# Kernel optimization log

Measured on AMD Instinct MI355X. Metric: run time of the kernel, lower is better.

The kernel has to match this reference:

```python
import jax, jax.numpy as jnp
from jax import lax
import numpy as np


def _bn(x, g, b, eps=1e-5):
    # BatchNorm2d in training mode: biased batch stats over (N,H,W) per channel
    m = jnp.mean(x, axis=(0, 2, 3), keepdims=True)
    v = jnp.mean((x - m) ** 2, axis=(0, 2, 3), keepdims=True)
    return (x - m) * lax.rsqrt(v + eps) * g[None, :, None, None] + b[None, :, None, None]


def _conv(x, w, b, pad):
    y = lax.conv_general_dilated(x, w, (1, 1), [(pad, pad), (pad, pad)],
                                 dimension_numbers=('NCHW', 'OIHW', 'NCHW'))
    return y + b[None, :, None, None]


def _prelu(x, a):
    return jnp.where(x >= 0, x, a * x)


def _maxpool2(x):
    return lax.reduce_window(x, -jnp.inf, lax.max, (1, 1, 2, 2), (1, 1, 2, 2), 'VALID')


def _up2(x):
    # UpsamplingBilinear2d(scale_factor=2) -> bilinear, align_corners=True
    B, C, H, W = x.shape
    def idx(n):
        pos = jnp.arange(2 * n, dtype=x.dtype) * (n - 1) / (2 * n - 1)
        lo = jnp.floor(pos).astype(jnp.int32)
        hi = jnp.minimum(lo + 1, n - 1)
        return lo, hi, pos - lo.astype(x.dtype)
    lo, hi, f = idx(H)
    x = x[:, :, lo, :] * (1 - f)[:, None] + x[:, :, hi, :] * f[:, None]
    lo, hi, f = idx(W)
    x = x[:, :, :, lo] * (1 - f) + x[:, :, :, hi] * f
    return x


def _forward(x, n16, sigma16, bias16, prelu_a,
             bn3_g, bn3_b, bn32_g, bn32_b, bn64_g, bn64_b, bn128_g, bn128_b,
             w1, b1, w2, b2, w3, b3, w4, b4, w5, b5, w6, b6, w7, b7, w11, b11):
    B, C, H, W = x.shape
    # 16 enhancement curves fused: r_k = x^{n_k} / (x^{n_k} + sigma_k^{n_k} + bias_k)
    xn = x[None] ** n16[:, None, None, None, None]          # (16,B,3,H,W)
    r = xn / (xn + (sigma16 ** n16)[:, None, None, None, None]
              + bias16[:, None, None, None, None])
    # each branch gets its own BatchNorm2d(3) stats (same affine params)
    r = jax.vmap(lambda t: _bn(t, bn3_g, bn3_b))(r)
    x_fusion = jnp.transpose(r, (1, 0, 2, 3, 4)).reshape(B, 16 * C, H, W)
    x1 = _bn(_maxpool2(_prelu(_conv(x_fusion, w1, b1, 1), prelu_a)), bn32_g, bn32_b)
    x2 = _bn(_maxpool2(_prelu(_conv(x1, w2, b2, 1), prelu_a)), bn64_g, bn64_b)
    x3 = _bn(_maxpool2(_prelu(_conv(x2, w3, b3, 1), prelu_a)), bn128_g, bn128_b)
    x4 = _bn(_conv(x3, w4, b4, 1), bn128_g, bn128_b)
    x5 = _bn(_up2(_prelu(_conv(jnp.concatenate([x4, x3], 1), w5, b5, 1), prelu_a)), bn64_g, bn64_b)
    x6 = _bn(_up2(_prelu(_conv(jnp.concatenate([x2, x5], 1), w6, b6, 1), prelu_a)), bn32_g, bn32_b)
    x_out = jax.nn.sigmoid(_up2(_prelu(_conv(jnp.concatenate([x1, x6], 1), w7, b7, 1), prelu_a)))
    x_out = _conv(x_out, w11, b11, 0)
    x_mean = jnp.mean(x, axis=1, keepdims=True)
    x_out1 = jnp.mean(x_out, axis=1, keepdims=True)
    return x_out1 * (x / (x_mean + 1e-6))


def setup_inputs() -> dict:
    key = jax.random.key(0)
    ks = jax.random.split(key, 16)
    B, H, W = 8, 256, 256
    nf = 32
    x = jax.random.uniform(ks[0], (B, 3, H, W), jnp.float32, 1e-3, 1.0)
    n16 = jnp.arange(1, 17, dtype=jnp.float32) * 0.5
    sigma16 = jnp.full((16,), 0.5, jnp.float32)
    bias16 = jnp.full((16,), 1e-4, jnp.float32)
    prelu_a = jnp.float32(0.25)
    def cw(k, o, i, kk):
        return jax.random.normal(k, (o, i, kk, kk), jnp.float32) * 0.05
    def cb(o):
        return jnp.zeros((o,), jnp.float32)
    return dict(
        x=x, n16=n16, sigma16=sigma16, bias16=bias16, prelu_a=prelu_a,
        bn3_g=jnp.ones((3,), jnp.float32), bn3_b=jnp.zeros((3,), jnp.float32),
        bn32_g=jnp.ones((32,), jnp.float32), bn32_b=jnp.zeros((32,), jnp.float32),
        bn64_g=jnp.ones((64,), jnp.float32), bn64_b=jnp.zeros((64,), jnp.float32),
        bn128_g=jnp.ones((128,), jnp.float32), bn128_b=jnp.zeros((128,), jnp.float32),
        w1=cw(ks[1], nf, 48, 3), b1=cb(nf),
        w2=cw(ks[2], 2 * nf, nf, 3), b2=cb(2 * nf),
        w3=cw(ks[3], 4 * nf, 2 * nf, 3), b3=cb(4 * nf),
        w4=cw(ks[4], 4 * nf, 4 * nf, 3), b4=cb(4 * nf),
        w5=cw(ks[5], 2 * nf, 8 * nf, 3), b5=cb(2 * nf),
        w6=cw(ks[6], nf, 4 * nf, 3), b6=cb(nf),
        w7=cw(ks[7], nf, 2 * nf, 3), b7=cb(nf),
        w11=cw(ks[8], 3, nf, 1), b11=cb(3),
    )


def reference(x, n16, sigma16, bias16, prelu_a,
              bn3_g, bn3_b, bn32_g, bn32_b, bn64_g, bn64_b, bn128_g, bn128_b,
              w1, b1, w2, b2, w3, b3, w4, b4, w5, b5, w6, b6, w7, b7, w11, b11):
    return _forward(x, n16, sigma16, bias16, prelu_a,
                    bn3_g, bn3_b, bn32_g, bn32_b, bn64_g, bn64_b, bn128_g, bn128_b,
                    w1, b1, w2, b2, w3, b3, w4, b4, w5, b5, w6, b6, w7, b7, w11, b11)
```

## Files before the change

kernel.cpp:

```cpp
#include <hip/hip_runtime.h>

#define FAST_EXP2(x) __builtin_amdgcn_exp2f(x)
#define FAST_LOG2(x) __builtin_amdgcn_logf(x)
#define FAST_RCP(x)  __builtin_amdgcn_rcpf(x)

static constexpr size_t S3_SUM=0,   S3_SQ=48;
static constexpr size_t S32A_SUM=96,  S32A_SQ=128;
static constexpr size_t S64A_SUM=160, S64A_SQ=224;
static constexpr size_t S128A_SUM=288,S128A_SQ=416;
static constexpr size_t S128B_SUM=544,S128B_SQ=672;
static constexpr size_t S64B_SUM=800, S64B_SQ=864;
static constexpr size_t S32B_SUM=928, S32B_SQ=960;
static constexpr size_t SPB_=2016, WBAR_=2032, BBAR_=2064;
static constexpr size_t T1_=4096;
static constexpr size_t T2_=T1_+4194304;
static constexpr size_t T3_=T2_+2097152;
static constexpr size_t T4_=T3_+1048576;
static constexpr size_t C5_=T4_+1048576;
static constexpr size_t U5_=C5_+524288;
static constexpr size_t C6_=U5_+2097152;
static constexpr size_t U6_=C6_+1048576;
static constexpr size_t C7_=U6_+4194304;
static constexpr size_t W1S_=C7_+4194304;
static constexpr size_t B1S_=W1S_+13824;
static constexpr size_t PAD_=B1S_+64;

__device__ inline void bn_ab(const float* __restrict__ sum, const float* __restrict__ sq,
                             const float* __restrict__ g, const float* __restrict__ bb,
                             float invN, int c, float& a, float& b)
{
    float m   = sum[c]*invN;
    float var = fmaxf(sq[c]*invN - m*m, 0.f);
    float inv = rsqrtf(var + 1e-5f);
    a = g[c]*inv;
    b = bb[c] - m*a;
}

__global__ __launch_bounds__(256) void k_branch_stats(
    const float* __restrict__ x, const float* __restrict__ n16,
    const float* __restrict__ sig16, const float* __restrict__ b16,
    float* __restrict__ sum, float* __restrict__ sq)
{
    const int c = blockIdx.x >> 9;
    const int chunk = blockIdx.x & 511;
    float nk[16], den[16];
#pragma unroll
    for (int k = 0; k < 16; ++k) { nk[k] = n16[k]; den[k] = powf(sig16[k], nk[k]) + b16[k]; }
    float s[16], q[16];
#pragma unroll
    for (int k = 0; k < 16; ++k) { s[k] = 0.f; q[k] = 0.f; }
    const int per = 1024;
    int start = chunk * per;
    for (int i = start + (int)threadIdx.x; i < start + per; i += 256) {
        int b = i >> 16, hw = i & 65535;
        float xv = x[(size_t)(b*3 + c)*65536 + hw];
        float t = FAST_LOG2(xv);
#pragma unroll
        for (int k = 0; k < 16; ++k) {
            float v = FAST_EXP2(nk[k]*t);
            float r = v * FAST_RCP(v + den[k]);
            s[k] += r; q[k] += r*r;
        }
    }
    __shared__ float red[4][32];
    int lane = threadIdx.x & 63, wid = threadIdx.x >> 6;
#pragma unroll
    for (int k = 0; k < 16; ++k) {
#pragma unroll
        for (int off = 32; off > 0; off >>= 1) {
            s[k] += __shfl_down(s[k], off);
            q[k] += __shfl_down(q[k], off);
        }
    }
    if (lane == 0) {
#pragma unroll
        for (int k = 0; k < 16; ++k) { red[wid][k] = s[k]; red[wid][16+k] = q[k]; }
    }
    __syncthreads();
    if (threadIdx.x < 32) {
        float v = red[0][threadIdx.x] + red[1][threadIdx.x] + red[2][threadIdx.x] + red[3][threadIdx.x];
        int k = threadIdx.x & 15;
        if (threadIdx.x < 16) atomicAdd(&sum[k*3 + c], v);
        else                  atomicAdd(&sq[k*3 + c], v);
    }
}

__global__ __launch_bounds__(256) void k_stats(
    const float* __restrict__ in, int C, int HW, int nchunks, int per,
    float* __restrict__ sum, float* __restrict__ sq)
{
    int c = blockIdx.x / nchunks;
    int chunk = blockIdx.x - c*nchunks;
    float s = 0.f, q = 0.f;
    int start = chunk * per, end = start + per;
    for (int i = start + (int)threadIdx.x; i < end; i += 256) {
        int b = i / HW, hw = i - b*HW;
        float v = in[((size_t)b*C + c)*HW + hw];
        s += v; q += v*v;
    }
#pragma unroll
    for (int off = 32; off > 0; off >>= 1) { s += __shfl_down(s, off); q += __shfl_down(q, off); }
    __shared__ float ss[4], qq[4];
    int lane = threadIdx.x & 63, wid = threadIdx.x >> 6;
    if (lane == 0) { ss[wid] = s; qq[wid] = q; }
    __syncthreads();
    if (threadIdx.x == 0) {
        atomicAdd(&sum[c], ss[0]+ss[1]+ss[2]+ss[3]);
        atomicAdd(&sq[c],  qq[0]+qq[1]+qq[2]+qq[3]);
    }
}

__global__ __launch_bounds__(256) void k_fill(
    float* __restrict__ out, const float* __restrict__ bias, int C, int HW, int total)
{
    int idx = blockIdx.x*256 + threadIdx.x;
    if (idx < total) {
        int c = (idx / HW) % C;
        out[idx] = bias[c];
    }
}

__global__ __launch_bounds__(256) void k_prep_all(
    const float* __restrict__ s3sum, const float* __restrict__ s3sq,
    const float* __restrict__ bn3_g, const float* __restrict__ bn3_b,
    const float* __restrict__ n16, const float* __restrict__ sig16, const float* __restrict__ b16,
    const float* __restrict__ w11, const float* __restrict__ b11,
    const float* __restrict__ w1, const float* __restrict__ b1,
    float* __restrict__ w1s, float* __restrict__ b1s, float* __restrict__ padg,
    float* __restrict__ spb, float* __restrict__ wbar, float* __restrict__ bbar)
{
    __shared__ float a3[48], b3[48];
    int tid = threadIdx.x;
    if (tid < 48) {
        float m   = s3sum[tid]*(1.f/524288.f);
        float var = fmaxf(s3sq[tid]*(1.f/524288.f) - m*m, 0.f);
        float inv = rsqrtf(var + 1e-5f);
        float a   = bn3_g[tid % 3]*inv;
        a3[tid] = a;
        b3[tid] = bn3_b[tid % 3] - m*a;
    }
    if (tid < 16) spb[tid] = powf(sig16[tid], n16[tid]) + b16[tid];
    else if (tid >= 64 && tid < 96) { int j = tid - 64; wbar[j] = (w11[j] + w11[32+j] + w11[64+j]) * (1.f/3.f); }
    else if (tid == 96) bbar[0] = (b11[0] + b11[1] + b11[2]) * (1.f/3.f);
    __syncthreads();
    if (tid < 48) padg[tid] = -b3[tid] * FAST_RCP(a3[tid]);
    for (int t = tid; t < 13824; t += 256) {
        int ci = (t / 9) % 48;
        w1s[t] = w1[t] * a3[ci];
    }
    if (tid < 32) {
        float s = b1[tid];
        const float* wp = w1 + tid*432;
        for (int i = 0; i < 432; ++i) s += wp[i] * b3[i/9];
        b1s[tid] = s;
    }
}

template<int COG>
__device__ inline void stats_reduceN(float (&ssum)[COG], float (&ssq)[COG],
                                     float (*redst)[2*COG], int cob,
                                     float* __restrict__ gsum, float* __restrict__ gsq)
{
    int lane = threadIdx.x & 63, wid = threadIdx.x >> 6;
#pragma unroll
    for (int co = 0; co < COG; ++co) {
#pragma unroll
        for (int off = 32; off > 0; off >>= 1) {
            ssum[co] += __shfl_down(ssum[co], off);
            ssq[co]  += __shfl_down(ssq[co],  off);
        }
    }
    if (lane == 0) {
#pragma unroll
        for (int co = 0; co < COG; ++co) { redst[wid][co] = ssum[co]; redst[wid][COG+co] = ssq[co]; }
    }
    __syncthreads();
    if (threadIdx.x < 2*COG) {
        float v = redst[0][threadIdx.x] + redst[1][threadIdx.x] + redst[2][threadIdx.x] + redst[3][threadIdx.x];
        if ((int)threadIdx.x < COG) atomicAdd(&gsum[cob + threadIdx.x], v);
        else                        atomicAdd(&gsq[cob + threadIdx.x - COG], v);
    }
}

template<int COG>
__global__ __launch_bounds__(256,2) void k_conv1f(
    const float* __restrict__ x,
    const float* __restrict__ n16, const float* __restrict__ spb,
    const float* __restrict__ w1s, const float* __restrict__ b1s,
    const float* __restrict__ padg,
    const float* __restrict__ prelu_a,
    float* __restrict__ out, float* __restrict__ gsum, float* __restrict__ gsq)
{
    const int tx = threadIdx.x & 15, ty = threadIdx.x >> 4;
    const int nco = 32 / COG;
    const int b = blockIdx.z / nco, cob = (blockIdx.z - b*nco)*COG;
    const int x0 = blockIdx.x*32, y0 = blockIdx.y*32;

    __shared__ float wl[COG*48*9];
    __shared__ float rl[2][3*1224];
    __shared__ float nl16[16], dl16[16], padl[48];
    __shared__ float redst[4][2*COG];

    for (int t = threadIdx.x; t < COG*48*9; t += 256) {
        int co = t % COG; int rest = t / COG;
        int kk = rest % 9; int ci = rest / 9;
        wl[t] = w1s[(((size_t)(cob+co))*48 + ci)*9 + kk];
    }
    if (threadIdx.x < 16)       nl16[threadIdx.x]    = n16[threadIdx.x];
    else if (threadIdx.x < 32)  dl16[threadIdx.x-16] = spb[threadIdx.x-16];
    else if (threadIdx.x < 80)  padl[threadIdx.x-32] = padg[threadIdx.x-32];

    float tlr[14];
    int off_[14]; int chpack = 0; int okf = 0;
#pragma unroll
    for (int j = 0; j < 14; ++j) {
        int i = threadIdx.x + 256*j;
        if (i < 3468) {
            int ch = i / 1156, jj = i - ch*1156;
            int rr = jj / 34, cc = jj - rr*34;
            int gy = y0 - 1 + rr, gx = x0 - 1 + cc;
            bool ok = (unsigned)gy < 256u && (unsigned)gx < 256u;
            off_[j] = ch*1224 + rr*36 + cc;
            chpack |= ch << (2*j);
            tlr[j] = 0.f;
            if (ok) {
                okf |= 1 << j;
                tlr[j] = FAST_LOG2(x[((size_t)(b*3+ch))*65536 + gy*256 + gx]);
            }
        } else { off_[j] = 3671; tlr[j] = 0.f; }
    }

    float acc[COG][4];
#pragma unroll
    for (int i = 0; i < COG; ++i)
#pragma unroll
        for (int j = 0; j < 4; ++j) acc[i][j] = 0.f;

    {
        float nk = nl16[0], dk = dl16[0];
#pragma unroll
        for (int j = 0; j < 14; ++j) {
            int ch = (chpack >> (2*j)) & 3;
            float pv = padl[ch];
            float v = FAST_EXP2(nk * tlr[j]);
            float rv = v * FAST_RCP(v + dk);
            rl[0][off_[j]] = ((okf >> j) & 1) ? rv : pv;
        }
    }
    __syncthreads();

#pragma unroll 1
    for (int k = 0; k < 16; ++k) {
        if (k < 15) {
            float nk = nl16[k+1], dk = dl16[k+1];
#pragma unroll
            for (int j = 0; j < 14; ++j) {
                int ch = (chpack >> (2*j)) & 3;
                float pv = padl[(k+1)*3 + ch];
                float v = FAST_EXP2(nk * tlr[j]);
                float rv = v * FAST_RCP(v + dk);
                rl[(k+1)&1][off_[j]] = ((okf >> j) & 1) ? rv : pv;
            }
        }
        const float* rbuf = rl[k&1];
#pragma unroll
        for (int ch = 0; ch < 3; ++ch) {
            const float* tlp = rbuf + ch*1224 + (2*ty)*36 + 2*tx;
            float iv[4][4];
#pragma unroll
            for (int r = 0; r < 4; ++r) {
                float2 a2 = *(const float2*)(tlp + r*36);
                float2 b2 = *(const float2*)(tlp + r*36 + 2);
                iv[r][0]=a2.x; iv[r][1]=a2.y; iv[r][2]=b2.x; iv[r][3]=b2.y;
            }
            const float* wbase = &wl[((k*3+ch)*9)*COG];
#pragma unroll
            for (int kh = 0; kh < 3; ++kh)
#pragma unroll
            for (int kw = 0; kw < 3; ++kw) {
                const int kk = kh*3 + kw;
                float wv[COG];
#pragma unroll
                for (int q = 0; q < COG/4; ++q) {
                    float4 wq = *((const float4*)(wbase + kk*COG) + q);
                    wv[4*q+0]=wq.x; wv[4*q+1]=wq.y; wv[4*q+2]=wq.z; wv[4*q+3]=wq.w;
                }
#pragma unroll
                for (int co = 0; co < COG; ++co)
#pragma unroll
                    for (int py = 0; py < 2; ++py)
#pragma unroll
                        for (int px = 0; px < 2; ++px)
                            acc[co][py*2+px] += wv[co]*iv[py+kh][px+kw];
            }
        }
        __syncthreads();
    }

    float a = __ldg(prelu_a);
    int pyp = (y0 >> 1) + ty, pxp = (x0 >> 1) + tx;
    float ssum[COG], ssq[COG];
#pragma unroll
    for (int co = 0; co < COG; ++co) {
        float bv = b1s[cob + co];
        float v0 = acc[co][0] + bv, v1 = acc[co][1] + bv;
        float v2 = acc[co][2] + bv, v3 = acc[co][3] + bv;
        v0 = v0 >= 0.f ? v0 : a*v0; v1 = v1 >= 0.f ? v1 : a*v1;
        v2 = v2 >= 0.f ? v2 : a*v2; v3 = v3 >= 0.f ? v3 : a*v3;
        float m = fmaxf(fmaxf(v0,v1), fmaxf(v2,v3));
        out[(((size_t)b*32 + cob + co)*128 + pyp)*128 + pxp] = m;
        ssum[co] = m; ssq[co] = m*m;
    }
    __syncthreads();
    stats_reduceN<COG>(ssum, ssq, redst, cob, gsum, gsq);
}

template<int COG, int MAXCI, bool POOL, bool SPLIT, bool STATS>
__global__ __launch_bounds__(256, (COG<=8) ? 4 : 2) void k_conv32(
    const float* __restrict__ in1, int C1,
    const float* __restrict__ sum1, const float* __restrict__ sq1,
    const float* __restrict__ g1, const float* __restrict__ bb1, float invN1,
    const float* __restrict__ in2, int C2,
    const float* __restrict__ sum2, const float* __restrict__ sq2,
    const float* __restrict__ g2, const float* __restrict__ bb2, float invN2,
    const float* __restrict__ w, const float* __restrict__ bias,
    int Cout, int H, int W, const float* __restrict__ prelu_a, int do_prelu,
    int ciN, int nsplit,
    float* __restrict__ out, float* __restrict__ gsum, float* __restrict__ gsq)
{
    const int Cin = C1 + C2;
    const int tx = threadIdx.x & 15, ty = threadIdx.x >> 4;
    const int nco = Cout / COG;
    int z = blockIdx.z;
    const int sp = z % nsplit; z /= nsplit;
    const int b = z / nco, cob = (z - b*nco)*COG;
    const int ci0 = sp * ciN;
    const int x0 = blockIdx.x*32, y0 = blockIdx.y*32;

    __shared__ float wl[COG*MAXCI*9];
    __shared__ float tile[2][34*36];
    __shared__ float redst[4][2*COG];

    for (int t = threadIdx.x; t < COG*ciN*9; t += 256) {
        int co = t % COG; int rest = t / COG;
        int k = rest % 9; int ci = rest / 9;
        wl[t] = w[(((size_t)(cob+co))*Cin + ci0 + ci)*9 + k];
    }

    float acc[COG][4];
#pragma unroll
    for (int i = 0; i < COG; ++i)
#pragma unroll
        for (int j = 0; j < 4; ++j) acc[i][j] = 0.f;

#pragma unroll 1
    for (int cb = 0; cb < ciN; cb += 2) {
#pragma unroll
        for (int sub = 0; sub < 2; ++sub) {
            int ci = ci0 + cb + sub;
            const float* in; int cc; int Cn;
            const float* sm; const float* sqp; const float* gg; const float* bbp; float iN;
            if (ci < C1) { in = in1; cc = ci;      Cn = C1; sm = sum1; sqp = sq1; gg = g1; bbp = bb1; iN = invN1; }
            else         { in = in2; cc = ci - C1; Cn = C2; sm = sum2; sqp = sq2; gg = g2; bbp = bb2; iN = invN2; }
            float scv = 1.f, shv = 0.f;
            if (sm) bn_ab(sm, sqp, gg, bbp, iN, cc, scv, shv);
            const float* base = in + ((size_t)b*Cn + cc)*H*W;
#pragma unroll 1
            for (int i = threadIdx.x; i < 34*34; i += 256) {
                int r = i / 34, c = i - r*34;
                int gy = y0 - 1 + r, gx = x0 - 1 + c;
                float v = 0.f;
                if ((unsigned)gy < (unsigned)H && (unsigned)gx < (unsigned)W)
                    v = base[(size_t)gy*W + gx]*scv + shv;
                tile[sub][r*36 + c] = v;
            }
        }
        __syncthreads();
#pragma unroll
        for (int sub = 0; sub < 2; ++sub) {
            const float* tl = &tile[sub][(2*ty)*36 + 2*tx];
            float iv[4][4];
#pragma unroll
            for (int r = 0; r < 4; ++r) {
                float2 a2 = *(const float2*)(tl + r*36);
                float2 b2 = *(const float2*)(tl + r*36 + 2);
                iv[r][0]=a2.x; iv[r][1]=a2.y; iv[r][2]=b2.x; iv[r][3]=b2.y;
            }
            const float* wbase = &wl[(cb+sub)*9*COG];
#pragma unroll
            for (int kh = 0; kh < 3; ++kh)
#pragma unroll
            for (int kw = 0; kw < 3; ++kw) {
                const int k = kh*3 + kw;
                float wv[COG];
#pragma unroll
                for (int q = 0; q < COG/4; ++q) {
                    float4 wq = *((const float4*)(wbase + k*COG) + q);
                    wv[4*q+0]=wq.x; wv[4*q+1]=wq.y; wv[4*q+2]=wq.z; wv[4*q+3]=wq.w;
                }
#pragma unroll
                for (int co = 0; co < COG; ++co)
#pragma unroll
                    for (int py = 0; py < 2; ++py)
#pragma unroll
                        for (int px = 0; px < 2; ++px)
                            acc[co][py*2+px] += wv[co]*iv[py+kh][px+kw];
            }
        }
        __syncthreads();
    }

    if (SPLIT) {
        int oy = y0 + 2*ty, ox = x0 + 2*tx;
#pragma unroll
        for (int co = 0; co < COG; ++co) {
            float* op = out + (((size_t)b*Cout + cob + co)*H + oy)*W + ox;
            atomicAdd(&op[0],     acc[co][0]);
            atomicAdd(&op[1],     acc[co][1]);
            atomicAdd(&op[W],     acc[co][2]);
            atomicAdd(&op[W + 1], acc[co][3]);
        }
    } else {
        float a = __ldg(prelu_a);
        float ssum[COG], ssq[COG];
        if (POOL) {
            const int Hp = H >> 1, Wp = W >> 1;
            int pyp = (y0 >> 1) + ty, pxp = (x0 >> 1) + tx;
#pragma unroll
            for (int co = 0; co < COG; ++co) {
                float bv = bias[cob + co];
                float v0 = acc[co][0] + bv, v1 = acc[co][1] + bv;
                float v2 = acc[co][2] + bv, v3 = acc[co][3] + bv;
                v0 = v0 >= 0.f ? v0 : a*v0; v1 = v1 >= 0.f ? v1 : a*v1;
                v2 = v2 >= 0.f ? v2 : a*v2; v3 = v3 >= 0.f ? v3 : a*v3;
                float m = fmaxf(fmaxf(v0,v1), fmaxf(v2,v3));
                out[(((size_t)b*Cout + cob + co)*Hp + pyp)*Wp + pxp] = m;
                ssum[co] = m; ssq[co] = m*m;
            }
            if (STATS) stats_reduceN<COG>(ssum, ssq, redst, cob, gsum, gsq);
        } else {
            int oy = y0 + 2*ty, ox = x0 + 2*tx;
#pragma unroll
            for (int co = 0; co < COG; ++co) {
                float bv = bias[cob + co];
                float* op = out + (((size_t)b*Cout + cob + co)*H + oy)*W + ox;
                float v0 = acc[co][0] + bv, v1 = acc[co][1] + bv;
                float v2 = acc[co][2] + bv, v3 = acc[co][3] + bv;
                if (do_prelu) {
                    v0 = v0 >= 0.f ? v0 : a*v0; v1 = v1 >= 0.f ? v1 : a*v1;
                    v2 = v2 >= 0.f ? v2 : a*v2; v3 = v3 >= 0.f ? v3 : a*v3;
                }
                op[0] = v0; op[1] = v1; op[W] = v2; op[W+1] = v3;
                ssum[co] = v0+v1+v2+v3; ssq[co] = v0*v0+v1*v1+v2*v2+v3*v3;
            }
            if (STATS) stats_reduceN<COG>(ssum, ssq, redst, cob, gsum, gsq);
        }
    }
}

__global__ __launch_bounds__(256) void k_up2(
    const float* __restrict__ in, float* __restrict__ out, int C, int h, int w,
    const float* __restrict__ prelu_a, int do_prelu,
    float* __restrict__ gsum, float* __restrict__ gsq)
{
    int idx = blockIdx.x*256 + threadIdx.x;
    int W2 = 2*w, H2 = 2*h;
    float a = do_prelu ? __ldg(prelu_a) : 0.f;
    int ox = idx % W2; int t = idx / W2; int oy = t % H2; int bc = t / H2;
    float py = ((float)oy * (float)(h-1)) / (float)(2*h - 1);
    int ly = (int)floorf(py); int hy = min(ly+1, h-1); float fy = py - (float)ly;
    float px = ((float)ox * (float)(w-1)) / (float)(2*w - 1);
    int lx = (int)floorf(px); int hx = min(lx+1, w-1); float fx = px - (float)lx;
    const float* p = in + (size_t)bc*h*w;
    float v00 = p[(size_t)ly*w + lx], v01 = p[(size_t)ly*w + hx];
    float v10 = p[(size_t)hy*w + lx], v11 = p[(size_t)hy*w + hx];
    if (do_prelu) {
        v00 = v00 >= 0.f ? v00 : a*v00;
        v01 = v01 >= 0.f ? v01 : a*v01;
        v10 = v10 >= 0.f ? v10 : a*v10;
        v11 = v11 >= 0.f ? v11 : a*v11;
    }
    float v0 = v00*(1.f-fx) + v01*fx;
    float v1 = v10*(1.f-fx) + v11*fx;
    float v = v0*(1.f-fy) + v1*fy;
    out[idx] = v;
    float s = v, q = v*v;
#pragma unroll
    for (int off = 32; off > 0; off >>= 1) { s += __shfl_down(s, off); q += __shfl_down(q, off); }
    __shared__ float ss[4], qq[4];
    int lane = threadIdx.x & 63, wid = threadIdx.x >> 6;
    if (lane == 0) { ss[wid] = s; qq[wid] = q; }
    __syncthreads();
    if (threadIdx.x == 0) {
        int c = bc % C;
        atomicAdd(&gsum[c], ss[0]+ss[1]+ss[2]+ss[3]);
        atomicAdd(&gsq[c],  qq[0]+qq[1]+qq[2]+qq[3]);
    }
}

__global__ __launch_bounds__(256) void k_final(
    const float* __restrict__ c7, const float* __restrict__ x,
    const float* __restrict__ wbar, const float* __restrict__ bbar,
    float* __restrict__ out)
{
    int idx = blockIdx.x*256 + threadIdx.x;
    if (idx >= 8*65536) return;
    int hw = idx & 65535, b = idx >> 16;
    int oy = hw >> 8, ox = hw & 255;
    float py = ((float)oy * 127.f) / 255.f;
    int ly = (int)floorf(py); int hy = min(ly+1, 127); float fy = py - (float)ly;
    float px = ((float)ox * 127.f) / 255.f;
    int lx = (int)floorf(px); int hx = min(lx+1, 127); float fx = px - (float)lx;
    float w00 = (1.f-fy)*(1.f-fx), w01 = (1.f-fy)*fx, w10 = fy*(1.f-fx), w11v = fy*fx;
    const float* base = c7 + (size_t)b*32*16384;
    float accum = bbar[0];
#pragma unroll 8
    for (int j = 0; j < 32; ++j) {
        const float* p = base + (size_t)j*16384;
        float v = p[ly*128 + lx]*w00 + p[ly*128 + hx]*w01 + p[hy*128 + lx]*w10 + p[hy*128 + hx]*w11v;
        float s = FAST_RCP(1.f + __expf(-v));
        accum += wbar[j]*s;
    }
    size_t xb = (size_t)b*3*65536 + hw;
    float x0 = x[xb], x1 = x[xb + 65536], x2 = x[xb + 2*65536];
    float m = (x0 + x1 + x2)*(1.f/3.f) + 1e-6f;
    float sc = accum * FAST_RCP(m);
    out[xb]            = sc*x0;
    out[xb + 65536]    = sc*x1;
    out[xb + 2*65536]  = sc*x2;
}

extern "C" void kernel_launch(void* const* d_in, const int* in_sizes, int n_in,
                              void* d_out, int out_size, void* d_ws, size_t ws_size,
                              hipStream_t stream) {
    const float* x       = (const float*)d_in[0];
    const float* n16     = (const float*)d_in[1];
    const float* sig16   = (const float*)d_in[2];
    const float* bia16   = (const float*)d_in[3];
    const float* prelu_a = (const float*)d_in[4];
    const float* bn3_g   = (const float*)d_in[5];
    const float* bn3_b   = (const float*)d_in[6];
    const float* bn32_g  = (const float*)d_in[7];
    const float* bn32_b  = (const float*)d_in[8];
    const float* bn64_g  = (const float*)d_in[9];
    const float* bn64_b  = (const float*)d_in[10];
    const float* bn128_g = (const float*)d_in[11];
    const float* bn128_b = (const float*)d_in[12];
    const float* w1 = (const float*)d_in[13]; const float* b1 = (const float*)d_in[14];
    const float* w2 = (const float*)d_in[15]; const float* b2 = (const float*)d_in[16];
    const float* w3 = (const float*)d_in[17]; const float* b3 = (const float*)d_in[18];
    const float* w4 = (const float*)d_in[19]; const float* b4 = (const float*)d_in[20];
    const float* w5 = (const float*)d_in[21]; const float* b5 = (const float*)d_in[22];
    const float* w6 = (const float*)d_in[23]; const float* b6 = (const float*)d_in[24];
    const float* w7 = (const float*)d_in[25]; const float* b7 = (const float*)d_in[26];
    const float* w11= (const float*)d_in[27]; const float* b11= (const float*)d_in[28];
    float* ws  = (float*)d_ws;
    float* out = (float*)d_out;

    (void)hipMemsetAsync(d_ws, 0, 4096*sizeof(float), stream);

    k_branch_stats<<<1536, 256, 0, stream>>>(x, n16, sig16, bia16, ws+S3_SUM, ws+S3_SQ);
    k_prep_all<<<1, 256, 0, stream>>>(ws+S3_SUM, ws+S3_SQ, bn3_g, bn3_b, n16, sig16, bia16,
                                      w11, b11, w1, b1,
                                      ws+W1S_, ws+B1S_, ws+PAD_, ws+SPB_, ws+WBAR_, ws+BBAR_);

    k_conv1f<8><<<dim3(8,8,32), 256, 0, stream>>>(x, n16, ws+SPB_, ws+W1S_, ws+B1S_, ws+PAD_,
                                                  prelu_a, ws+T1_, ws+S32A_SUM, ws+S32A_SQ);

    k_conv32<16,32,true,false,true><<<dim3(4,4,32), 256, 0, stream>>>(
        ws+T1_, 32, ws+S32A_SUM, ws+S32A_SQ, bn32_g, bn32_b, 1.f/131072.f,
        nullptr, 0, nullptr, nullptr, nullptr, nullptr, 0.f,
        w2, b2, 64, 128, 128, prelu_a, 1, 32, 1, ws+T2_, ws+S64A_SUM, ws+S64A_SQ);

    k_conv32<8,64,true,false,true><<<dim3(2,2,128), 256, 0, stream>>>(
        ws+T2_, 64, ws+S64A_SUM, ws+S64A_SQ, bn64_g, bn64_b, 1.f/32768.f,
        nullptr, 0, nullptr, nullptr, nullptr, nullptr, 0.f,
        w3, b3, 128, 64, 64, prelu_a, 1, 64, 1, ws+T3_, ws+S128A_SUM, ws+S128A_SQ);

    k_fill<<<4096, 256, 0, stream>>>(ws+T4_, b4, 128, 1024, 1048576);
    k_conv32<8,16,false,true,false><<<dim3(1,1,1024), 256, 0, stream>>>(
        ws+T3_, 128, ws+S128A_SUM, ws+S128A_SQ, bn128_g, bn128_b, 1.f/8192.f,
        nullptr, 0, nullptr, nullptr, nullptr, nullptr, 0.f,
        w4, nullptr, 128, 32, 32, prelu_a, 0, 16, 8, ws+T4_, nullptr, nullptr);
    k_stats<<<512, 256, 0, stream>>>(ws+T4_, 128, 1024, 4, 2048, ws+S128B_SUM, ws+S128B_SQ);

    k_fill<<<2048, 256, 0, stream>>>(ws+C5_, b5, 64, 1024, 524288);
    k_conv32<8,16,false,true,false><<<dim3(1,1,1024), 256, 0, stream>>>(
        ws+T4_, 128, ws+S128B_SUM, ws+S128B_SQ, bn128_g, bn128_b, 1.f/8192.f,
        ws+T3_, 128, ws+S128A_SUM, ws+S128A_SQ, bn128_g, bn128_b, 1.f/8192.f,
        w5, nullptr, 64, 32, 32, prelu_a, 0, 16, 16, ws+C5_, nullptr, nullptr);
    k_up2<<<8192, 256, 0, stream>>>(ws+C5_, ws+U5_, 64, 32, 32, prelu_a, 1, ws+S64B_SUM, ws+S64B_SQ);

    k_fill<<<4096, 256, 0, stream>>>(ws+C6_, b6, 32, 4096, 1048576);
    k_conv32<8,16,false,true,false><<<dim3(2,2,256), 256, 0, stream>>>(
        ws+T2_, 64, ws+S64A_SUM, ws+S64A_SQ, bn64_g, bn64_b, 1.f/32768.f,
        ws+U5_, 64, ws+S64B_SUM, ws+S64B_SQ, bn64_g, bn64_b, 1.f/32768.f,
        w6, nullptr, 32, 64, 64, prelu_a, 0, 16, 8, ws+C6_, nullptr, nullptr);
    k_up2<<<16384, 256, 0, stream>>>(ws+C6_, ws+U6_, 32, 64, 64, prelu_a, 1, ws+S32B_SUM, ws+S32B_SQ);

    k_conv32<8,64,false,false,false><<<dim3(4,4,32), 256, 0, stream>>>(
        ws+T1_, 32, ws+S32A_SUM, ws+S32A_SQ, bn32_g, bn32_b, 1.f/131072.f,
        ws+U6_, 32, ws+S32B_SUM, ws+S32B_SQ, bn32_g, bn32_b, 1.f/131072.f,
        w7, b7, 32, 128, 128, prelu_a, 1, 64, 1, ws+C7_, nullptr, nullptr);

    k_final<<<2048, 256, 0, stream>>>(ws+C7_, x, ws+WBAR_, ws+BBAR_, out);
}
```

Measured before the change: 1.360 ms.

## Double-buffer conv input tiles with register staging to overlap loads and compute

```diff
diff --git a/kernel.cpp b/kernel.cpp
--- a/kernel.cpp
+++ b/kernel.cpp
@@ -316,7 +316,7 @@
 }
 
 template<int COG, int MAXCI, bool POOL, bool SPLIT, bool STATS>
-__global__ __launch_bounds__(256, (COG<=8) ? 4 : 2) void k_conv32(
+__global__ __launch_bounds__(256, (COG<=8) ? 3 : 2) void k_conv32(
     const float* __restrict__ in1, int C1,
     const float* __restrict__ sum1, const float* __restrict__ sq1,
     const float* __restrict__ g1, const float* __restrict__ bb1, float invN1,
@@ -338,7 +338,7 @@
     const int x0 = blockIdx.x*32, y0 = blockIdx.y*32;
 
     __shared__ float wl[COG*MAXCI*9];
-    __shared__ float tile[2][34*36];
+    __shared__ float tile[2][2][34*36];
     __shared__ float redst[4][2*COG];
 
     for (int t = threadIdx.x; t < COG*ciN*9; t += 256) {
@@ -347,14 +347,22 @@
         wl[t] = w[(((size_t)(cob+co))*Cin + ci0 + ci)*9 + k];
     }
 
-    float acc[COG][4];
-#pragma unroll
-    for (int i = 0; i < COG; ++i)
-#pragma unroll
-        for (int j = 0; j < 4; ++j) acc[i][j] = 0.f;
-
-#pragma unroll 1
-    for (int cb = 0; cb < ciN; cb += 2) {
+    int goff[5];
+    int loff[5];
+#pragma unroll
+    for (int s = 0; s < 5; ++s) {
+        int i = threadIdx.x + 256*s;
+        goff[s] = -2; loff[s] = 0;
+        if (i < 1156) {
+            int r = i / 34, c = i - r*34;
+            loff[s] = r*36 + c;
+            int gy = y0 - 1 + r, gx = x0 - 1 + c;
+            goff[s] = ((unsigned)gy < (unsigned)H && (unsigned)gx < (unsigned)W) ? gy*W + gx : -1;
+        }
+    }
+
+    float stg[2][5];
+    auto load_chunk = [&](int cb) {
 #pragma unroll
         for (int sub = 0; sub < 2; ++sub) {
             int ci = ci0 + cb + sub;
@@ -365,20 +373,40 @@
             float scv = 1.f, shv = 0.f;
             if (sm) bn_ab(sm, sqp, gg, bbp, iN, cc, scv, shv);
             const float* base = in + ((size_t)b*Cn + cc)*H*W;
+#pragma unroll
+            for (int s = 0; s < 5; ++s) {
+                float v = 0.f;
+                if (goff[s] >= 0) v = base[goff[s]]*scv + shv;
+                stg[sub][s] = v;
+            }
+        }
+    };
+    auto write_chunk = [&](int buf) {
+#pragma unroll
+        for (int sub = 0; sub < 2; ++sub)
+#pragma unroll
+            for (int s = 0; s < 5; ++s)
+                if (goff[s] != -2) tile[buf][sub][loff[s]] = stg[sub][s];
+    };
+
+    float acc[COG][4];
+#pragma unroll
+    for (int i = 0; i < COG; ++i)
+#pragma unroll
+        for (int j = 0; j < 4; ++j) acc[i][j] = 0.f;
+
+    load_chunk(0);
+    write_chunk(0);
+    __syncthreads();
+
+    int buf = 0;
 #pragma unroll 1
-            for (int i = threadIdx.x; i < 34*34; i += 256) {
-                int r = i / 34, c = i - r*34;
-                int gy = y0 - 1 + r, gx = x0 - 1 + c;
-                float v = 0.f;
-                if ((unsigned)gy < (unsigned)H && (unsigned)gx < (unsigned)W)
-                    v = base[(size_t)gy*W + gx]*scv + shv;
-                tile[sub][r*36 + c] = v;
-            }
-        }
-        __syncthreads();
+    for (int cb = 0; cb < ciN; cb += 2) {
+        const bool hasnext = (cb + 2) < ciN;
+        if (hasnext) load_chunk(cb + 2);
 #pragma unroll
         for (int sub = 0; sub < 2; ++sub) {
-            const float* tl = &tile[sub][(2*ty)*36 + 2*tx];
+            const float* tl = &tile[buf][sub][(2*ty)*36 + 2*tx];
             float iv[4][4];
 #pragma unroll
             for (int r = 0; r < 4; ++r) {
@@ -407,7 +435,9 @@
                             acc[co][py*2+px] += wv[co]*iv[py+kh][px+kw];
             }
         }
+        if (hasnext) write_chunk(buf ^ 1);
         __syncthreads();
+        buf ^= 1;
     }
 
     if (SPLIT) {
```

Measured after the change: 3.976 ms. +192.4%, slower.
